# Optimization experiments

Hardware: AMD Instinct MI355X
Metric: run time of the kernel (lower is better)

The kernel has to match this reference:

```python
import jax, jax.numpy as jnp
import numpy as np

B, S, D, H, N = 2, 2048, 768, 12, 128  # batch, seq_len, d_model, n_heads, num_segments
EPS_LN = 1e-5


def _layer_norm(x, g, b):
    m = x.mean(-1, keepdims=True)
    v = ((x - m) ** 2).mean(-1, keepdims=True)
    return (x - m) / jnp.sqrt(v + EPS_LN) * g + b


def _mha(q, k, v, Wqkv, bqkv, Wo, bo, n_heads):
    """torch.nn.MultiheadAttention (batch_first), returns (out, head-averaged attn)."""
    d = q.shape[-1]
    dh = d // n_heads
    Wq, Wk, Wv = jnp.split(Wqkv, 3, axis=0)
    bq, bk, bv = jnp.split(bqkv, 3)
    qh = (q @ Wq.T + bq).reshape(q.shape[0], q.shape[1], n_heads, dh)
    kh = (k @ Wk.T + bk).reshape(k.shape[0], k.shape[1], n_heads, dh)
    vh = (v @ Wv.T + bv).reshape(v.shape[0], v.shape[1], n_heads, dh)
    scores = jnp.einsum('bqhd,bkhd->bhqk', qh, kh) / jnp.sqrt(jnp.asarray(dh, q.dtype))
    attn = jax.nn.softmax(scores, axis=-1)                      # [B,H,Sq,Sk]
    out = jnp.einsum('bhqk,bkhd->bqhd', attn, vh).reshape(q.shape[0], q.shape[1], d)
    return out @ Wo.T + bo, attn.mean(axis=1)                   # attn avg over heads


def _aggregate(x, w, seg):  # per-batch: weighted mean of tokens into N segments
    num = jax.ops.segment_sum(w[:, None] * x, seg, num_segments=N)
    den = jax.ops.segment_sum(w, seg, num_segments=N)
    return num / (den[:, None] + 1e-8)


def setup_inputs() -> dict:
    key = jax.random.key(0)
    ks = jax.random.split(key, 16)
    s = 0.02
    inp = {
        'hidden_states': jax.random.normal(ks[0], (B, S, D), jnp.float32),
        'token_to_segment': jnp.sort(jax.random.randint(ks[1], (B, S), 0, N), axis=-1),
        # token_attention (shared for node-level self-attn in the adjacency=None branch)
        'Wqkv_t': jax.random.normal(ks[2], (3 * D, D), jnp.float32) * s,
        'bqkv_t': jnp.zeros((3 * D,), jnp.float32),
        'Wo_t': jax.random.normal(ks[3], (D, D), jnp.float32) * s,
        'bo_t': jnp.zeros((D,), jnp.float32),
        # cross_attention
        'Wqkv_c': jax.random.normal(ks[4], (3 * D, D), jnp.float32) * s,
        'bqkv_c': jnp.zeros((3 * D,), jnp.float32),
        'Wo_c': jax.random.normal(ks[5], (D, D), jnp.float32) * s,
        'bo_c': jnp.zeros((D,), jnp.float32),
        # layer norms
        'g_tok': jnp.ones((D,), jnp.float32),
        'b_tok': jnp.zeros((D,), jnp.float32),
        'g_node': jnp.ones((D,), jnp.float32),
        'b_node': jnp.zeros((D,), jnp.float32),
        # output projection
        'W_out': jax.random.normal(ks[6], (D, D), jnp.float32) * s,
        'b_out': jnp.zeros((D,), jnp.float32),
    }
    return inp


def reference(hidden_states, token_to_segment, Wqkv_t, bqkv_t, Wo_t, bo_t,
              Wqkv_c, bqkv_c, Wo_c, bo_c, g_tok, b_tok, g_node, b_node,
              W_out, b_out):
    hs = hidden_states
    # token-level self-attention + residual norm
    tok_attn_out, tok_attn = _mha(hs, hs, hs, Wqkv_t, bqkv_t, Wo_t, bo_t, H)
    token_output = _layer_norm(hs + tok_attn_out, g_tok, b_tok)
    # token -> node attention-weighted scatter aggregation
    w = tok_attn.mean(axis=1)  # [B,S] attention received per token
    node_emb = jax.vmap(_aggregate)(token_output, w, token_to_segment)  # [B,N,D]
    # node-level self-attention (reuses token_attention weights; adjacency=None path)
    node_out, node_attn = _mha(node_emb, node_emb, node_emb, Wqkv_t, bqkv_t, Wo_t, bo_t, H)
    node_emb = _layer_norm(node_emb + node_out, g_node, b_node)
    # cross-attention: tokens attend to nodes
    cross_out, cross_w = _mha(token_output, node_emb, node_emb, Wqkv_c, bqkv_c, Wo_c, bo_c, H)
    token_output = token_output + cross_out
    # node -> token gather + additive combine
    gathered = jnp.take_along_axis(node_emb, token_to_segment[:, :, None], axis=1)  # [B,S,D]
    enhanced = token_output + gathered
    output = enhanced @ W_out.T + b_out
    return output, node_emb, tok_attn, node_attn, cross_w
```

## Files before the change

### kernel.cpp

```cpp
#include <hip/hip_runtime.h>
#include <cstdint>

#define B_ 2
#define S_ 2048
#define D_ 768
#define H_ 12
#define DH_ 64
#define N_ 128

typedef unsigned short u16;
typedef unsigned int u32;
typedef unsigned long long u64;
typedef __attribute__((ext_vector_type(8))) short short8;
typedef __attribute__((ext_vector_type(4))) float f32x4;

#define MFMA16(a, b, c) __builtin_amdgcn_mfma_f32_16x16x32_bf16(a, b, c, 0, 0, 0)

__device__ inline u16 f2bf(float f) {
  union { float f; u32 u; } v; v.f = f;
  u32 r = v.u + 0x7FFFu + ((v.u >> 16) & 1u);
  return (u16)(r >> 16);
}
__device__ inline u32 pk2(float a, float b) {
  return (u32)f2bf(a) | ((u32)f2bf(b) << 16);
}
__device__ inline u32 cvtpk(float lo, float hi) {
  u32 r;
  asm("v_cvt_pk_bf16_f32 %0, %1, %2" : "=v"(r) : "v"(lo), "v"(hi));
  return r;
}
__device__ inline float bf2f(u16 h) {
  union { u32 u; float f; } v; v.u = ((u32)h) << 16;
  return v.f;
}
__device__ inline float wredmax(float v) {
  #pragma unroll
  for (int o = 32; o > 0; o >>= 1) v = fmaxf(v, __shfl_down(v, o));
  return v;
}
__device__ inline float wredsum(float v) {
  #pragma unroll
  for (int o = 32; o > 0; o >>= 1) v += __shfl_down(v, o);
  return v;
}
__device__ inline void async_lds16(const u16* g, u16* l) {
  __builtin_amdgcn_global_load_lds((const __attribute__((address_space(1))) void*)g,
                                   (__attribute__((address_space(3))) void*)l, 16, 0, 0);
}

__global__ void conv_bf16(const float* __restrict__ in, u16* __restrict__ outp, int n8) {
  int i = blockIdx.x * 256 + threadIdx.x;
  if (i >= n8) return;
  const float4* p = (const float4*)(in + (size_t)i * 8);
  float4 a = p[0], b = p[1];
  uint4 u;
  u.x = pk2(a.x, a.y); u.y = pk2(a.z, a.w); u.z = pk2(b.x, b.y); u.w = pk2(b.z, b.w);
  *(uint4*)(outp + (size_t)i * 8) = u;
}

template <int OUT_BF16>
__global__ __launch_bounds__(256) void gemm_bf16(
    const u16* __restrict__ A, int lda,
    const u16* __restrict__ W, int ldb,
    const float* __restrict__ bias,
    void* __restrict__ Cout, int ldc, int K) {
  __shared__ u16 As[128 * 32];
  __shared__ u16 Ws[128 * 32];
  const int tid = threadIdx.x;
  const int m0 = blockIdx.y * 128, n0 = blockIdx.x * 128;
  const int w = tid >> 6, lane = tid & 63;
  const int msub = (w & 1) * 64, nsub = (w >> 1) * 64;
  const int lrow = lane & 15, quad = lane >> 4;
  const int e0 = tid * 8;
  const int r0 = e0 >> 5, c0 = e0 & 31;
  const int e1 = e0 + 2048;
  const int r1 = e1 >> 5, c1 = e1 & 31;
  const u16* Ag0 = A + (size_t)(m0 + r0) * lda + c0;
  const u16* Ag1 = A + (size_t)(m0 + r1) * lda + c1;
  const u16* Wg0 = W + (size_t)(n0 + r0) * ldb + c0;
  const u16* Wg1 = W + (size_t)(n0 + r1) * ldb + c1;
  u16* AsB0 = As + (w << 9);
  u16* AsB1 = As + 2048 + (w << 9);
  u16* WsB0 = Ws + (w << 9);
  u16* WsB1 = Ws + 2048 + (w << 9);
  f32x4 zero = {0.f, 0.f, 0.f, 0.f};
  f32x4 acc[4][4];
  #pragma unroll
  for (int i = 0; i < 4; i++)
    #pragma unroll
    for (int j = 0; j < 4; j++) acc[i][j] = zero;
  for (int k0 = 0; k0 < K; k0 += 32) {
    __syncthreads();
    async_lds16(Ag0 + k0, AsB0);
    async_lds16(Ag1 + k0, AsB1);
    async_lds16(Wg0 + k0, WsB0);
    async_lds16(Wg1 + k0, WsB1);
    __syncthreads();
    short8 af[4], bf[4];
    #pragma unroll
    for (int i = 0; i < 4; i++)
      af[i] = *(const short8*)(As + (msub + i * 16 + lrow) * 32 + quad * 8);
    #pragma unroll
    for (int j = 0; j < 4; j++)
      bf[j] = *(const short8*)(Ws + (nsub + j * 16 + lrow) * 32 + quad * 8);
    #pragma unroll
    for (int i = 0; i < 4; i++)
      #pragma unroll
      for (int j = 0; j < 4; j++)
        acc[i][j] = MFMA16(af[i], bf[j], acc[i][j]);
  }
  #pragma unroll
  for (int i = 0; i < 4; i++) {
    #pragma unroll
    for (int j = 0; j < 4; j++) {
      int col = n0 + nsub + j * 16 + lrow;
      float bv = bias ? bias[col] : 0.f;
      #pragma unroll
      for (int r = 0; r < 4; r++) {
        int row = m0 + msub + i * 16 + quad * 4 + r;
        float val = acc[i][j][r] + bv;
        if (OUT_BF16) ((u16*)Cout)[(size_t)row * ldc + col] = f2bf(val);
        else ((float*)Cout)[(size_t)row * ldc + col] = val;
      }
    }
  }
}

__global__ __launch_bounds__(256) void transpose_v(const u16* __restrict__ qkv, u16* __restrict__ VT) {
  __shared__ u16 t[64][72];
  const int z = blockIdx.y, b = z / 12, h = z - b * 12;
  const int s0 = blockIdx.x * 64;
  const int tid = threadIdx.x;
  {
    int r = tid >> 2, dp = (tid & 3) * 16;
    const u16* src = qkv + (size_t)b * 2048 * 2304 + (size_t)(s0 + r) * 2304 + 1536 + h * 64 + dp;
    *(uint4*)&t[r][dp] = *(const uint4*)src;
    *(uint4*)&t[r][dp + 8] = *(const uint4*)(src + 8);
  }
  __syncthreads();
  int d = tid >> 2, sp = (tid & 3) * 16;
  u16 vals[16];
  #pragma unroll
  for (int i = 0; i < 16; i++) vals[i] = t[sp + i][d];
  u16* dst = VT + ((size_t)z * 64 + d) * 2048 + s0 + sp;
  *(uint4*)dst = *(uint4*)&vals[0];
  *(uint4*)(dst + 8) = *(uint4*)&vals[8];
}

__global__ __launch_bounds__(512) void fused_tok_attn(
    const u16* __restrict__ qkv, const u16* __restrict__ VT,
    float* __restrict__ amF, u16* __restrict__ amH, u16* __restrict__ attnout) {
  __shared__ u16 pbuf[8 * 2 * 16 * 264];
  __shared__ float lred[8][2][16];
  __shared__ float obuf[2][2][16][66];
  const int tid = threadIdx.x;
  const int w = tid >> 6, lane = tid & 63;
  const int lrow = lane & 15, quad = lane >> 4;
  const int lid = blockIdx.x;
  const int xcd = lid & 7;
  const int combo = xcd >> 1;
  const int b = combo >> 1, z = combo & 1;
  const int q0 = (((lid >> 3) << 1) + (xcd & 1)) << 5;
  const int h0 = z * 6;
  const u16* qp = qkv + (size_t)b * 2048 * 2304;
  const u16* kp = qp + 768;
  const int strip = w * 256;
  const int jj = w & 3, sh = w >> 2;
  u16* ob = attnout + (size_t)b * 2048 * 768 + (size_t)q0 * 768;
  u16* pbA = pbuf + (w * 2 + 0) * 16 * 264;
  u16* pbB = pbuf + (w * 2 + 1) * 16 * 264;
  f32x4 zero = {0.f, 0.f, 0.f, 0.f};
  float amreg[2][8][8];
  #pragma unroll
  for (int g = 0; g < 2; g++)
    #pragma unroll
    for (int c = 0; c < 8; c++)
      #pragma unroll
      for (int e = 0; e < 8; e++) amreg[g][c][e] = 0.f;
  for (int hh = 0; hh < 6; hh++) {
    const int h = h0 + hh;
    const u16* qhA = qp + (size_t)(q0 + lrow) * 2304 + h * 64 + quad * 8;
    const u16* qhB = qp + (size_t)(q0 + 16 + lrow) * 2304 + h * 64 + quad * 8;
    short8 qfA0 = *(const short8*)qhA;
    short8 qfA1 = *(const short8*)(qhA + 32);
    short8 qfB0 = *(const short8*)qhB;
    short8 qfB1 = *(const short8*)(qhB + 32);
    float lsumA = 0.f, lsumB = 0.f;
    #pragma unroll
    for (int t = 0; t < 16; t++) {
      const u16* kh = kp + (size_t)(strip + t * 16 + lrow) * 2304 + h * 64 + quad * 8;
      short8 kf0 = *(const short8*)kh;
      short8 kf1 = *(const short8*)(kh + 32);
      f32x4 svA = zero, svB = zero;
      svA = MFMA16(kf0, qfA0, svA);
      svA = MFMA16(kf1, qfA1, svA);
      svB = MFMA16(kf0, qfB0, svB);
      svB = MFMA16(kf1, qfB1, svB);
      float a0 = __expf(svA[0] * 0.125f);
      float a1 = __expf(svA[1] * 0.125f);
      float a2 = __expf(svA[2] * 0.125f);
      float a3 = __expf(svA[3] * 0.125f);
      float b0 = __expf(svB[0] * 0.125f);
      float b1 = __expf(svB[1] * 0.125f);
      float b2 = __expf(svB[2] * 0.125f);
      float b3 = __expf(svB[3] * 0.125f);
      lsumA += (a0 + a1) + (a2 + a3);
      lsumB += (b0 + b1) + (b2 + b3);
      u32 wA0 = cvtpk(a0, a1), wA1 = cvtpk(a2, a3);
      u32 wB0 = cvtpk(b0, b1), wB1 = cvtpk(b2, b3);
      *(u64*)(pbA + lrow * 264 + t * 16 + quad * 4) = (u64)wA0 | ((u64)wA1 << 32);
      *(u64*)(pbB + lrow * 264 + t * 16 + quad * 4) = (u64)wB0 | ((u64)wB1 << 32);
    }
    lsumA += __shfl_xor(lsumA, 16);
    lsumA += __shfl_xor(lsumA, 32);
    lsumB += __shfl_xor(lsumB, 16);
    lsumB += __shfl_xor(lsumB, 32);
    if (lane < 16) { lred[w][0][lane] = lsumA; lred[w][1][lane] = lsumB; }
    __syncthreads();
    float invqA, invqB;
    float inv4A[4], inv4B[4];
    {
      float sA = 0.f, sB = 0.f;
      #pragma unroll
      for (int w2 = 0; w2 < 8; w2++) { sA += lred[w2][0][lrow]; sB += lred[w2][1][lrow]; }
      invqA = 1.f / sA; invqB = 1.f / sB;
      #pragma unroll
      for (int r = 0; r < 4; r++) {
        float rA = 0.f, rB = 0.f;
        #pragma unroll
        for (int w2 = 0; w2 < 8; w2++) {
          rA += lred[w2][0][quad * 4 + r];
          rB += lred[w2][1][quad * 4 + r];
        }
        inv4A[r] = 1.f / rA; inv4B[r] = 1.f / rB;
      }
    }
    #pragma unroll
    for (int c = 0; c < 8; c++) {
      short8 pfa = *(const short8*)(pbA + lrow * 264 + c * 32 + quad * 8);
      short8 pfb = *(const short8*)(pbB + lrow * 264 + c * 32 + quad * 8);
      #pragma unroll
      for (int e = 0; e < 8; e++) {
        amreg[0][c][e] += bf2f((u16)pfa[e]) * invqA;
        amreg[1][c][e] += bf2f((u16)pfb[e]) * invqB;
      }
    }
    f32x4 oA = zero, oB = zero;
    {
      const u16* vtp = VT + (size_t)(b * 12 + h) * 64 * 2048;
      const u16* vbase = vtp + (size_t)(jj * 16 + lrow) * 2048 + sh * 1024 + quad * 8;
      #pragma unroll
      for (int cc = 0; cc < 32; cc++) {
        short8 vf = *(const short8*)(vbase + cc * 32);
        const u16* pba = pbuf + (((4 * sh + (cc >> 3)) * 2 + 0) * 16 * 264) + lrow * 264 + (cc & 7) * 32 + quad * 8;
        const u16* pbb = pba + 16 * 264;
        oA = MFMA16(*(const short8*)pba, vf, oA);
        oB = MFMA16(*(const short8*)pbb, vf, oB);
      }
    }
    #pragma unroll
    for (int r = 0; r < 4; r++) {
      obuf[0][sh][quad * 4 + r][jj * 16 + lrow] = oA[r] * inv4A[r];
      obuf[1][sh][quad * 4 + r][jj * 16 + lrow] = oB[r] * inv4B[r];
    }
    __syncthreads();
    #pragma unroll
    for (int ee = 0; ee < 4; ee++) {
      int e2 = tid + ee * 512;
      int row = e2 >> 6, col = e2 & 63;
      int g = row >> 4, rr = row & 15;
      float s = obuf[g][0][rr][col] + obuf[g][1][rr][col];
      ob[(size_t)row * 768 + h * 64 + col] = f2bf(s);
    }
  }
  if (z == 0) {
    #pragma unroll
    for (int g = 0; g < 2; g++) {
      float* ar = amF + ((size_t)b * 2048 + q0 + g * 16 + lrow) * 2048 + strip;
      #pragma unroll
      for (int c = 0; c < 8; c++) {
        float4 v0 = {amreg[g][c][0], amreg[g][c][1], amreg[g][c][2], amreg[g][c][3]};
        float4 v1 = {amreg[g][c][4], amreg[g][c][5], amreg[g][c][6], amreg[g][c][7]};
        *(float4*)(ar + c * 32 + quad * 8) = v0;
        *(float4*)(ar + c * 32 + quad * 8 + 4) = v1;
      }
    }
  } else {
    #pragma unroll
    for (int g = 0; g < 2; g++) {
      u16* ar = amH + ((size_t)b * 2048 + q0 + g * 16 + lrow) * 2048 + strip;
      #pragma unroll
      for (int c = 0; c < 8; c++) {
        uint4 u;
        u.x = pk2(amreg[g][c][0], amreg[g][c][1]);
        u.y = pk2(amreg[g][c][2], amreg[g][c][3]);
        u.z = pk2(amreg[g][c][4], amreg[g][c][5]);
        u.w = pk2(amreg[g][c][6], amreg[g][c][7]);
        *(uint4*)(ar + c * 32 + quad * 8) = u;
      }
    }
  }
}

__global__ void combine_am(float* __restrict__ amF, const u16* __restrict__ amH) {
  size_t i = ((size_t)blockIdx.x * 256 + threadIdx.x) * 8;
  float4 a0 = *(float4*)(amF + i);
  float4 a1 = *(float4*)(amF + i + 4);
  uint4 hb = *(const uint4*)(amH + i);
  const float c12 = 1.f / 12.f;
  float4 r0, r1;
  r0.x = (a0.x + bf2f((u16)(hb.x & 0xffff))) * c12;
  r0.y = (a0.y + bf2f((u16)(hb.x >> 16))) * c12;
  r0.z = (a0.z + bf2f((u16)(hb.y & 0xffff))) * c12;
  r0.w = (a0.w + bf2f((u16)(hb.y >> 16))) * c12;
  r1.x = (a1.x + bf2f((u16)(hb.z & 0xffff))) * c12;
  r1.y = (a1.y + bf2f((u16)(hb.z >> 16))) * c12;
  r1.z = (a1.z + bf2f((u16)(hb.w & 0xffff))) * c12;
  r1.w = (a1.w + bf2f((u16)(hb.w >> 16))) * c12;
  *(float4*)(amF + i) = r0;
  *(float4*)(amF + i + 4) = r1;
}

__global__ __launch_bounds__(256) void qk_mfma(
    const u16* __restrict__ Q, int ldq, long qbs,
    const u16* __restrict__ Kp, int ldk, long kbs,
    float* __restrict__ S, long szs, int Sk, int nh, float scale) {
  __shared__ u16 Qs[128 * 72];
  __shared__ u16 Ks[128 * 72];
  const int tid = threadIdx.x;
  const int z = blockIdx.z, bb = z / nh, h = z - bb * nh;
  const u16* qp = Q + (size_t)bb * qbs + h * 64;
  const u16* kp = Kp + (size_t)bb * kbs + h * 64;
  float* sp = S + (size_t)z * szs;
  const int m0 = blockIdx.y * 128, n0 = blockIdx.x * 128;
  const int w = tid >> 6, lane = tid & 63;
  const int msub = (w & 1) * 64, nsub = (w >> 1) * 64;
  const int lrow = lane & 15, quad = lane >> 4;
  const int srow = tid >> 1, shalf = tid & 1;
  {
    const uint4* qg = (const uint4*)(qp + (size_t)(m0 + srow) * ldq + shalf * 32);
    const uint4* kg = (const uint4*)(kp + (size_t)(n0 + srow) * ldk + shalf * 32);
    uint4* qd = (uint4*)(Qs + srow * 72 + shalf * 32);
    uint4* kd = (uint4*)(Ks + srow * 72 + shalf * 32);
    #pragma unroll
    for (int u = 0; u < 4; u++) { qd[u] = qg[u]; kd[u] = kg[u]; }
  }
  __syncthreads();
  f32x4 zero = {0.f, 0.f, 0.f, 0.f};
  f32x4 acc[4][4];
  #pragma unroll
  for (int i = 0; i < 4; i++)
    #pragma unroll
    for (int j = 0; j < 4; j++) acc[i][j] = zero;
  #pragma unroll
  for (int ks = 0; ks < 2; ks++) {
    short8 af[4], bf[4];
    #pragma unroll
    for (int i = 0; i < 4; i++)
      af[i] = *(const short8*)(Qs + (msub + i * 16 + lrow) * 72 + ks * 32 + quad * 8);
    #pragma unroll
    for (int j = 0; j < 4; j++)
      bf[j] = *(const short8*)(Ks + (nsub + j * 16 + lrow) * 72 + ks * 32 + quad * 8);
    #pragma unroll
    for (int i = 0; i < 4; i++)
      #pragma unroll
      for (int j = 0; j < 4; j++)
        acc[i][j] = MFMA16(af[i], bf[j], acc[i][j]);
  }
  #pragma unroll
  for (int i = 0; i < 4; i++)
    #pragma unroll
    for (int j = 0; j < 4; j++) {
      int col = n0 + nsub + j * 16 + lrow;
      #pragma unroll
      for (int r = 0; r < 4; r++) {
        int row = m0 + msub + i * 16 + quad * 4 + r;
        sp[(size_t)row * Sk + col] = acc[i][j][r] * scale;
      }
    }
}

__global__ __launch_bounds__(128) void softmax_small(
    float* __restrict__ Sc, float* __restrict__ wout, int Sq) {
  const int q = blockIdx.x, b = blockIdx.y, tid = threadIdx.x;
  const int w = tid >> 6, lane = tid & 63;
  __shared__ float red[2];
  float am = 0.f;
  const size_t plane = (size_t)Sq * 128;
  for (int h = 0; h < 12; h++) {
    const int z = b * 12 + h;
    float* row = Sc + (size_t)z * plane + (size_t)q * 128;
    float v = row[tid];
    float m = wredmax(v);
    if (lane == 0) red[w] = m;
    __syncthreads();
    m = fmaxf(red[0], red[1]);
    float e = __expf(v - m);
    float s = wredsum(e);
    __syncthreads();
    if (lane == 0) red[w] = s;
    __syncthreads();
    float p = e / (red[0] + red[1]);
    ((u16*)(Sc + (size_t)z * plane))[(size_t)q * 256 + tid] = f2bf(p);
    am += p;
    __syncthreads();
  }
  wout[((size_t)b * Sq + q) * 128 + tid] = am * (1.f / 12.f);
}

__global__ __launch_bounds__(256) void pv_small(
    const u16* __restrict__ Pb, long pzs,
    const u16* __restrict__ KVb, int ldv, long vbs, int vhoff,
    u16* __restrict__ Outb, long obs) {
  __shared__ u16 Ps[128 * 40];
  __shared__ u16 Vs[64 * 40];
  const int tid = threadIdx.x;
  const int z = blockIdx.y, b = z / 12, h = z - b * 12;
  const u16* Pp = Pb + (size_t)z * pzs;
  const u16* Vp = KVb + (size_t)b * vbs + vhoff + h * 64;
  u16* Op = Outb + (size_t)b * obs + h * 64;
  const int m0 = blockIdx.x * 128;
  const int w = tid >> 6, lane = tid & 63;
  const int msub = w * 32;
  const int lrow = lane & 15, quad = lane >> 4;
  const int srow = tid >> 1, shalf = tid & 1;
  const int vk = tid >> 3, vn = (tid & 7) * 8;
  f32x4 zero = {0.f, 0.f, 0.f, 0.f};
  f32x4 acc[2][4];
  #pragma unroll
  for (int i = 0; i < 2; i++)
    #pragma unroll
    for (int j = 0; j < 4; j++) acc[i][j] = zero;
  #pragma unroll
  for (int k0 = 0; k0 < 128; k0 += 32) {
    uint4 pa = *(const uint4*)(Pp + (size_t)(m0 + srow) * 256 + k0 + shalf * 16);
    uint4 pb2 = *(const uint4*)(Pp + (size_t)(m0 + srow) * 256 + k0 + shalf * 16 + 8);
    uint4 vv = *(const uint4*)(Vp + (size_t)(k0 + vk) * ldv + vn);
    __syncthreads();
    *(uint4*)(Ps + srow * 40 + shalf * 16) = pa;
    *(uint4*)(Ps + srow * 40 + shalf * 16 + 8) = pb2;
    const u16* vs = (const u16*)&vv;
    #pragma unroll
    for (int u = 0; u < 8; u++) Vs[(vn + u) * 40 + vk] = vs[u];
    __syncthreads();
    short8 af[2], bf[4];
    #pragma unroll
    for (int i = 0; i < 2; i++)
      af[i] = *(const short8*)(Ps + (msub + i * 16 + lrow) * 40 + quad * 8);
    #pragma unroll
    for (int j = 0; j < 4; j++)
      bf[j] = *(const short8*)(Vs + (j * 16 + lrow) * 40 + quad * 8);
    #pragma unroll
    for (int i = 0; i < 2; i++)
      #pragma unroll
      for (int j = 0; j < 4; j++)
        acc[i][j] = MFMA16(af[i], bf[j], acc[i][j]);
  }
  #pragma unroll
  for (int i = 0; i < 2; i++)
    #pragma unroll
    for (int j = 0; j < 4; j++) {
      int col = j * 16 + lrow;
      #pragma unroll
      for (int r = 0; r < 4; r++) {
        int row = m0 + msub + i * 16 + quad * 4 + r;
        Op[(size_t)row * D_ + col] = f2bf(acc[i][j][r]);
      }
    }
}

__global__ void ln_kernel(const float* __restrict__ x1, const float* __restrict__ x2,
                          const float* __restrict__ g, const float* __restrict__ bt,
                          float* __restrict__ outp, u16* __restrict__ outbf) {
  const int row = blockIdx.x;
  const int tid = threadIdx.x;
  __shared__ float red[8];
  float v[3];
  #pragma unroll
  for (int j = 0; j < 3; j++) {
    int c = tid + j * 256;
    v[j] = x1[(size_t)row * D_ + c] + x2[(size_t)row * D_ + c];
  }
  float s = v[0] + v[1] + v[2];
  s = wredsum(s);
  int wid = tid >> 6, lane = tid & 63;
  if (lane == 0) red[wid] = s;
  __syncthreads();
  float mean = (red[0] + red[1] + red[2] + red[3]) / 768.f;
  float d0 = v[0] - mean, d1 = v[1] - mean, d2 = v[2] - mean;
  float q = d0 * d0 + d1 * d1 + d2 * d2;
  q = wredsum(q);
  if (lane == 0) red[4 + wid] = q;
  __syncthreads();
  float var = (red[4] + red[5] + red[6] + red[7]) / 768.f;
  float inv = rsqrtf(var + 1e-5f);
  #pragma unroll
  for (int j = 0; j < 3; j++) {
    int c = tid + j * 256;
    float val = (v[j] - mean) * inv * g[c] + bt[c];
    outp[(size_t)row * D_ + c] = val;
    if (outbf) outbf[(size_t)row * D_ + c] = f2bf(val);
  }
}

__global__ void colmean_part(const float* __restrict__ ta, float* __restrict__ part) {
  int b = blockIdx.y, z = blockIdx.z;
  int k = blockIdx.x * 256 + threadIdx.x;
  const float* p = ta + (size_t)b * S_ * S_ + (size_t)z * 256 * S_ + k;
  float s = 0.f;
  #pragma unroll 8
  for (int q = 0; q < 256; q++) s += p[(size_t)q * S_];
  part[((size_t)z * B_ + b) * S_ + k] = s;
}

__global__ void colmean_final(const float* __restrict__ part, float* __restrict__ w) {
  int b = blockIdx.y;
  int k = blockIdx.x * 256 + threadIdx.x;
  float s = 0.f;
  #pragma unroll
  for (int z = 0; z < 8; z++) s += part[((size_t)z * B_ + b) * S_ + k];
  w[b * S_ + k] = s * (1.f / (float)S_);
}

__global__ void aggregate_kernel(const float* __restrict__ x, const float* __restrict__ w,
                                 const int* __restrict__ seg, float* __restrict__ outp,
                                 u16* __restrict__ outbf) {
  const int b = blockIdx.y, n = blockIdx.x;
  const int* sg = seg + b * S_;
  int l = 0, rr = S_;
  while (l < rr) { int mid = (l + rr) >> 1; if (sg[mid] < n) l = mid + 1; else rr = mid; }
  const int lo = l;
  rr = S_;
  while (l < rr) { int mid = (l + rr) >> 1; if (sg[mid] < n + 1) l = mid + 1; else rr = mid; }
  const int hi = l;
  const int tid = threadIdx.x;
  float acc[3] = {0.f, 0.f, 0.f};
  float den = 0.f;
  for (int s = lo; s < hi; s++) {
    float ww = w[b * S_ + s];
    den += ww;
    const float* xr = x + (size_t)(b * S_ + s) * D_;
    #pragma unroll
    for (int j = 0; j < 3; j++) acc[j] += ww * xr[tid + j * 256];
  }
  float invd = 1.f / (den + 1e-8f);
  size_t ro = (size_t)(b * N_ + n) * D_;
  #pragma unroll
  for (int j = 0; j < 3; j++) {
    float val = acc[j] * invd;
    outp[ro + tid + j * 256] = val;
    outbf[ro + tid + j * 256] = f2bf(val);
  }
}

__global__ void enhanced_kernel(const float* __restrict__ tokout, const float* __restrict__ crossp,
                                const float* __restrict__ nodeemb, const int* __restrict__ seg,
                                u16* __restrict__ outbf) {
  int g8 = blockIdx.x * 256 + threadIdx.x;
  int bs = g8 / 96, d0 = (g8 - bs * 96) * 8;
  int b = bs >> 11;
  int n = seg[bs];
  const float* t = tokout + (size_t)bs * D_ + d0;
  const float* cp = crossp + (size_t)bs * D_ + d0;
  const float* ne = nodeemb + (size_t)(b * N_ + n) * D_ + d0;
  float4 a0 = *(const float4*)t, a1 = *(const float4*)(t + 4);
  float4 b0 = *(const float4*)cp, b1 = *(const float4*)(cp + 4);
  float4 c0 = *(const float4*)ne, c1 = *(const float4*)(ne + 4);
  uint4 u;
  u.x = pk2(a0.x + b0.x + c0.x, a0.y + b0.y + c0.y);
  u.y = pk2(a0.z + b0.z + c0.z, a0.w + b0.w + c0.w);
  u.z = pk2(a1.x + b1.x + c1.x, a1.y + b1.y + c1.y);
  u.w = pk2(a1.z + b1.z + c1.z, a1.w + b1.w + c1.w);
  *(uint4*)(outbf + (size_t)g8 * 8) = u;
}

extern "C" void kernel_launch(void* const* d_in, const int* in_sizes, int n_in,
                              void* d_out, int out_size, void* d_ws, size_t ws_size,
                              hipStream_t stream) {
  const float* hs     = (const float*)d_in[0];
  const int*   t2s    = (const int*)d_in[1];
  const float* Wqkv_t = (const float*)d_in[2];
  const float* bqkv_t = (const float*)d_in[3];
  const float* Wo_t   = (const float*)d_in[4];
  const float* bo_t   = (const float*)d_in[5];
  const float* Wqkv_c = (const float*)d_in[6];
  const float* bqkv_c = (const float*)d_in[7];
  const float* Wo_c   = (const float*)d_in[8];
  const float* bo_c   = (const float*)d_in[9];
  const float* g_tok  = (const float*)d_in[10];
  const float* b_tok  = (const float*)d_in[11];
  const float* g_node = (const float*)d_in[12];
  const float* b_node = (const float*)d_in[13];
  const float* W_out  = (const float*)d_in[14];
  const float* b_out  = (const float*)d_in[15];

  float* ws = (float*)d_ws;
  u16*   qkvbf       = (u16*)ws;
  u16*   enh_bf      = (u16*)ws;
  u16*   crossqbf    = (u16*)(ws + 1572864);
  u16*   crossattn_bf= (u16*)(ws + 3145728);
  float* R1 = ws + 4718592;
  u16*   hs_bf   = (u16*)R1;
  u16*   wqkvt1  = (u16*)(R1 + 1572864);
  u16*   VT      = (u16*)R1;
  u16*   amh     = (u16*)(R1 + 4194304);
  float* projbuf = R1;
  float* Snode   = R1;
  u16*   wqkvt2  = (u16*)(R1 + 4000000);
  u16*   wot     = (u16*)(R1 + 6291456);
  u16*   wqkvc   = (u16*)R1;
  u16*   woc     = (u16*)(R1 + 6291456);
  u16*   wout    = (u16*)(R1 + 6586368);
  float* Scross  = R1;
  float* crossproj = R1;
  float* R2 = ws + 13107200;
  u16*   attnout_bf = (u16*)R2;
  u16*   tokout_bf  = (u16*)R2;
  float* wvec       = R2 + 1572864;
  float* colpart    = R2 + 1576960;
  float* nodepre    = R2 + 1609728;
  float* nodeproj   = R2 + 1806336;
  u16*   nodepre_bf = (u16*)(R2 + 2002944);
  u16*   nodeattn_bf= (u16*)(R2 + 2101248);
  u16*   nodeemb_bf = (u16*)(R2 + 2199552);
  u16*   nodeqkvbf  = (u16*)(R2 + 2297856);
  u16*   crosskvbf  = (u16*)(R2 + 2592768);
  float* tokout = ws + 16252928;

  float* outp       = (float*)d_out;
  float* o_output   = outp;
  float* o_nodeemb  = outp + 3145728;
  float* o_tokattn  = o_nodeemb + 196608;
  float* o_nodeattn = o_tokattn + 8388608;
  float* o_crossw   = o_nodeattn + 32768;

  conv_bf16<<<1536, 256, 0, stream>>>(hs, hs_bf, 393216);
  conv_bf16<<<864, 256, 0, stream>>>(Wqkv_t, wqkvt1, 221184);
  gemm_bf16<1><<<dim3(18, 32), 256, 0, stream>>>(hs_bf, 768, wqkvt1, 768, bqkv_t, qkvbf, 2304, 768);

  transpose_v<<<dim3(32, 24), 256, 0, stream>>>(qkvbf, VT);
  fused_tok_attn<<<256, 512, 0, stream>>>(qkvbf, VT, o_tokattn, amh, attnout_bf);
  combine_am<<<4096, 256, 0, stream>>>(o_tokattn, amh);

  conv_bf16<<<288, 256, 0, stream>>>(Wo_t, wot, 73728);
  gemm_bf16<0><<<dim3(6, 32), 256, 0, stream>>>(attnout_bf, 768, wot, 768, bo_t, projbuf, 768, 768);
  ln_kernel<<<4096, 256, 0, stream>>>(hs, projbuf, g_tok, b_tok, tokout, tokout_bf);

  colmean_part<<<dim3(8, 2, 8), 256, 0, stream>>>(o_tokattn, colpart);
  colmean_final<<<dim3(8, 2), 256, 0, stream>>>(colpart, wvec);
  aggregate_kernel<<<dim3(128, 2), 256, 0, stream>>>(tokout, wvec, t2s, nodepre, nodepre_bf);
  conv_bf16<<<864, 256, 0, stream>>>(Wqkv_t, wqkvt2, 221184);
  gemm_bf16<1><<<dim3(18, 2), 256, 0, stream>>>(nodepre_bf, 768, wqkvt2, 768, bqkv_t, nodeqkvbf, 2304, 768);
  qk_mfma<<<dim3(1, 1, 24), 256, 0, stream>>>(
      nodeqkvbf, 2304, (long)128 * 2304, nodeqkvbf + 768, 2304, (long)128 * 2304,
      Snode, 16384, 128, 12, 0.125f);
  softmax_small<<<dim3(128, 2), 128, 0, stream>>>(Snode, o_nodeattn, 128);
  pv_small<<<dim3(1, 24), 256, 0, stream>>>(
      (const u16*)Snode, 32768, nodeqkvbf, 2304, (long)128 * 2304, 1536,
      nodeattn_bf, (long)128 * 768);
  gemm_bf16<0><<<dim3(6, 2), 256, 0, stream>>>(nodeattn_bf, 768, wot, 768, bo_t, nodeproj, 768, 768);
  ln_kernel<<<256, 256, 0, stream>>>(nodepre, nodeproj, g_node, b_node, o_nodeemb, nodeemb_bf);

  conv_bf16<<<864, 256, 0, stream>>>(Wqkv_c, wqkvc, 221184);
  conv_bf16<<<288, 256, 0, stream>>>(Wo_c, woc, 73728);
  conv_bf16<<<288, 256, 0, stream>>>(W_out, wout, 73728);
  gemm_bf16<1><<<dim3(6, 32), 256, 0, stream>>>(tokout_bf, 768, wqkvc, 768, bqkv_c, crossqbf, 768, 768);
  gemm_bf16<1><<<dim3(12, 2), 256, 0, stream>>>(nodeemb_bf, 768, wqkvc + 768 * 768, 768, bqkv_c + 768,
                                                crosskvbf, 1536, 768);

  qk_mfma<<<dim3(1, 16, 24), 256, 0, stream>>>(
      crossqbf, 768, (long)2048 * 768, crosskvbf, 1536, (long)128 * 1536,
      Scross, 262144, 128, 12, 0.125f);
  softmax_small<<<dim3(2048, 2), 128, 0, stream>>>(Scross, o_crossw, 2048);
  pv_small<<<dim3(16, 24), 256, 0, stream>>>(
      (const u16*)Scross, 524288, crosskvbf, 1536, (long)128 * 1536, 768,
      crossattn_bf, (long)2048 * 768);

  gemm_bf16<0><<<dim3(6, 32), 256, 0, stream>>>(crossattn_bf, 768, woc, 768, bo_c, crossproj, 768, 768);
  enhanced_kernel<<<1536, 256, 0, stream>>>(tokout, crossproj, o_nodeemb, t2s, enh_bf);
  gemm_bf16<0><<<dim3(6, 32), 256, 0, stream>>>(enh_bf, 768, wout, 768, b_out, o_output, 768, 768);
}
```

Measured before the change: 556.9 us.

## Fuse small attention stages and fold head-average combine into column mean

Replaces the separate QK, softmax and PV kernels for node and cross attention with one attn_small kernel that keeps scores in registers and LDS and writes head-averaged weights directly. The combine pass over the token attention map is merged into the column-mean partial kernel, so the large fp32 map is read and written once fewer times. fused_tok_attn also gets a minimum-occupancy launch bound. The fused softmax omits the max subtraction, which risks overflow for large scores.

```diff
diff --git a/kernel.cpp b/kernel.cpp
--- a/kernel.cpp
+++ b/kernel.cpp
@@ -32,11 +32,6 @@
 __device__ inline float bf2f(u16 h) {
   union { u32 u; float f; } v; v.u = ((u32)h) << 16;
   return v.f;
-}
-__device__ inline float wredmax(float v) {
-  #pragma unroll
-  for (int o = 32; o > 0; o >>= 1) v = fmaxf(v, __shfl_down(v, o));
-  return v;
 }
 __device__ inline float wredsum(float v) {
   #pragma unroll
@@ -147,7 +142,7 @@
   *(uint4*)(dst + 8) = *(uint4*)&vals[8];
 }
 
-__global__ __launch_bounds__(512) void fused_tok_attn(
+__global__ __launch_bounds__(512, 2) void fused_tok_attn(
     const u16* __restrict__ qkv, const u16* __restrict__ VT,
     float* __restrict__ amF, u16* __restrict__ amH, u16* __restrict__ attnout) {
   __shared__ u16 pbuf[8 * 2 * 16 * 264];
@@ -302,171 +297,120 @@
   }
 }
 
-__global__ void combine_am(float* __restrict__ amF, const u16* __restrict__ amH) {
-  size_t i = ((size_t)blockIdx.x * 256 + threadIdx.x) * 8;
-  float4 a0 = *(float4*)(amF + i);
-  float4 a1 = *(float4*)(amF + i + 4);
-  uint4 hb = *(const uint4*)(amH + i);
+__global__ __launch_bounds__(256) void attn_small(
+    const u16* __restrict__ Qp, int ldq, long qbs,
+    const u16* __restrict__ Kp, int ldk, long kbs,
+    const u16* __restrict__ Vp,
+    u16* __restrict__ Outb, long obs,
+    float* __restrict__ wout, int Sq) {
+  __shared__ u16 pbuf[16][136];
+  __shared__ u16 Vs[64][136];
+  __shared__ float lred[4][16];
+  const int tid = threadIdx.x;
+  const int w = tid >> 6, lane = tid & 63;
+  const int lrow = lane & 15, quad = lane >> 4;
+  const int q0 = blockIdx.x * 16, b = blockIdx.y;
+  const u16* qb = Qp + (size_t)b * qbs;
+  const u16* kb = Kp + (size_t)b * kbs;
+  const u16* vb = Vp + (size_t)b * kbs;
+  u16* ob = Outb + (size_t)b * obs + (size_t)q0 * 768;
+  f32x4 zero = {0.f, 0.f, 0.f, 0.f};
+  float cw[2][4];
+  #pragma unroll
+  for (int t = 0; t < 2; t++)
+    #pragma unroll
+    for (int r = 0; r < 4; r++) cw[t][r] = 0.f;
+  for (int h = 0; h < 12; h++) {
+    __syncthreads();
+    #pragma unroll
+    for (int j = 0; j < 4; j++) {
+      int lin = tid * 32 + j * 8;
+      int s = lin >> 6, d = lin & 63;
+      uint4 vv = *(const uint4*)(vb + (size_t)s * ldk + h * 64 + d);
+      const u16* vsrc = (const u16*)&vv;
+      #pragma unroll
+      for (int u = 0; u < 8; u++) Vs[d + u][s] = vsrc[u];
+    }
+    const u16* qh = qb + (size_t)(q0 + lrow) * ldq + h * 64 + quad * 8;
+    short8 qf0 = *(const short8*)qh;
+    short8 qf1 = *(const short8*)(qh + 32);
+    float pr[2][4];
+    float lsum = 0.f;
+    #pragma unroll
+    for (int t = 0; t < 2; t++) {
+      const u16* kh = kb + (size_t)(w * 32 + t * 16 + lrow) * ldk + h * 64 + quad * 8;
+      short8 kf0 = *(const short8*)kh;
+      short8 kf1 = *(const short8*)(kh + 32);
+      f32x4 sv = zero;
+      sv = MFMA16(kf0, qf0, sv);
+      sv = MFMA16(kf1, qf1, sv);
+      #pragma unroll
+      for (int r = 0; r < 4; r++) {
+        float p = __expf(sv[r] * 0.125f);
+        pr[t][r] = p;
+        lsum += p;
+      }
+      u32 w0 = cvtpk(pr[t][0], pr[t][1]), w1 = cvtpk(pr[t][2], pr[t][3]);
+      *(u64*)(&pbuf[lrow][w * 32 + t * 16 + quad * 4]) = (u64)w0 | ((u64)w1 << 32);
+    }
+    lsum += __shfl_xor(lsum, 16);
+    lsum += __shfl_xor(lsum, 32);
+    if (lane < 16) lred[w][lane] = lsum;
+    __syncthreads();
+    float invq = 1.f / (lred[0][lrow] + lred[1][lrow] + lred[2][lrow] + lred[3][lrow]);
+    float inv4[4];
+    #pragma unroll
+    for (int r = 0; r < 4; r++)
+      inv4[r] = 1.f / (lred[0][quad * 4 + r] + lred[1][quad * 4 + r] +
+                       lred[2][quad * 4 + r] + lred[3][quad * 4 + r]);
+    #pragma unroll
+    for (int t = 0; t < 2; t++)
+      #pragma unroll
+      for (int r = 0; r < 4; r++) cw[t][r] += pr[t][r] * invq;
+    f32x4 oacc = zero;
+    #pragma unroll
+    for (int cc = 0; cc < 4; cc++) {
+      short8 pf = *(const short8*)(&pbuf[lrow][cc * 32 + quad * 8]);
+      short8 vf = *(const short8*)(&Vs[w * 16 + lrow][cc * 32 + quad * 8]);
+      oacc = MFMA16(pf, vf, oacc);
+    }
+    #pragma unroll
+    for (int r = 0; r < 4; r++)
+      ob[(size_t)(quad * 4 + r) * 768 + h * 64 + w * 16 + lrow] = f2bf(oacc[r] * inv4[r]);
+  }
+  float* wr = wout + ((size_t)b * Sq + q0 + lrow) * 128 + w * 32;
   const float c12 = 1.f / 12.f;
-  float4 r0, r1;
-  r0.x = (a0.x + bf2f((u16)(hb.x & 0xffff))) * c12;
-  r0.y = (a0.y + bf2f((u16)(hb.x >> 16))) * c12;
-  r0.z = (a0.z + bf2f((u16)(hb.y & 0xffff))) * c12;
-  r0.w = (a0.w + bf2f((u16)(hb.y >> 16))) * c12;
-  r1.x = (a1.x + bf2f((u16)(hb.z & 0xffff))) * c12;
-  r1.y = (a1.y + bf2f((u16)(hb.z >> 16))) * c12;
-  r1.z = (a1.z + bf2f((u16)(hb.w & 0xffff))) * c12;
-  r1.w = (a1.w + bf2f((u16)(hb.w >> 16))) * c12;
-  *(float4*)(amF + i) = r0;
-  *(float4*)(amF + i + 4) = r1;
-}
-
-__global__ __launch_bounds__(256) void qk_mfma(
-    const u16* __restrict__ Q, int ldq, long qbs,
-    const u16* __restrict__ Kp, int ldk, long kbs,
-    float* __restrict__ S, long szs, int Sk, int nh, float scale) {
-  __shared__ u16 Qs[128 * 72];
-  __shared__ u16 Ks[128 * 72];
-  const int tid = threadIdx.x;
-  const int z = blockIdx.z, bb = z / nh, h = z - bb * nh;
-  const u16* qp = Q + (size_t)bb * qbs + h * 64;
-  const u16* kp = Kp + (size_t)bb * kbs + h * 64;
-  float* sp = S + (size_t)z * szs;
-  const int m0 = blockIdx.y * 128, n0 = blockIdx.x * 128;
-  const int w = tid >> 6, lane = tid & 63;
-  const int msub = (w & 1) * 64, nsub = (w >> 1) * 64;
-  const int lrow = lane & 15, quad = lane >> 4;
-  const int srow = tid >> 1, shalf = tid & 1;
-  {
-    const uint4* qg = (const uint4*)(qp + (size_t)(m0 + srow) * ldq + shalf * 32);
-    const uint4* kg = (const uint4*)(kp + (size_t)(n0 + srow) * ldk + shalf * 32);
-    uint4* qd = (uint4*)(Qs + srow * 72 + shalf * 32);
-    uint4* kd = (uint4*)(Ks + srow * 72 + shalf * 32);
-    #pragma unroll
-    for (int u = 0; u < 4; u++) { qd[u] = qg[u]; kd[u] = kg[u]; }
-  }
-  __syncthreads();
-  f32x4 zero = {0.f, 0.f, 0.f, 0.f};
-  f32x4 acc[4][4];
-  #pragma unroll
-  for (int i = 0; i < 4; i++)
-    #pragma unroll
-    for (int j = 0; j < 4; j++) acc[i][j] = zero;
-  #pragma unroll
-  for (int ks = 0; ks < 2; ks++) {
-    short8 af[4], bf[4];
-    #pragma unroll
-    for (int i = 0; i < 4; i++)
-      af[i] = *(const short8*)(Qs + (msub + i * 16 + lrow) * 72 + ks * 32 + quad * 8);
-    #pragma unroll
-    for (int j = 0; j < 4; j++)
-      bf[j] = *(const short8*)(Ks + (nsub + j * 16 + lrow) * 72 + ks * 32 + quad * 8);
-    #pragma unroll
-    for (int i = 0; i < 4; i++)
-      #pragma unroll
-      for (int j = 0; j < 4; j++)
-        acc[i][j] = MFMA16(af[i], bf[j], acc[i][j]);
-  }
-  #pragma unroll
-  for (int i = 0; i < 4; i++)
-    #pragma unroll
-    for (int j = 0; j < 4; j++) {
-      int col = n0 + nsub + j * 16 + lrow;
-      #pragma unroll
-      for (int r = 0; r < 4; r++) {
-        int row = m0 + msub + i * 16 + quad * 4 + r;
-        sp[(size_t)row * Sk + col] = acc[i][j][r] * scale;
-      }
-    }
-}
-
-__global__ __launch_bounds__(128) void softmax_small(
-    float* __restrict__ Sc, float* __restrict__ wout, int Sq) {
-  const int q = blockIdx.x, b = blockIdx.y, tid = threadIdx.x;
-  const int w = tid >> 6, lane = tid & 63;
-  __shared__ float red[2];
-  float am = 0.f;
-  const size_t plane = (size_t)Sq * 128;
-  for (int h = 0; h < 12; h++) {
-    const int z = b * 12 + h;
-    float* row = Sc + (size_t)z * plane + (size_t)q * 128;
-    float v = row[tid];
-    float m = wredmax(v);
-    if (lane == 0) red[w] = m;
-    __syncthreads();
-    m = fmaxf(red[0], red[1]);
-    float e = __expf(v - m);
-    float s = wredsum(e);
-    __syncthreads();
-    if (lane == 0) red[w] = s;
-    __syncthreads();
-    float p = e / (red[0] + red[1]);
-    ((u16*)(Sc + (size_t)z * plane))[(size_t)q * 256 + tid] = f2bf(p);
-    am += p;
-    __syncthreads();
-  }
-  wout[((size_t)b * Sq + q) * 128 + tid] = am * (1.f / 12.f);
-}
-
-__global__ __launch_bounds__(256) void pv_small(
-    const u16* __restrict__ Pb, long pzs,
-    const u16* __restrict__ KVb, int ldv, long vbs, int vhoff,
-    u16* __restrict__ Outb, long obs) {
-  __shared__ u16 Ps[128 * 40];
-  __shared__ u16 Vs[64 * 40];
-  const int tid = threadIdx.x;
-  const int z = blockIdx.y, b = z / 12, h = z - b * 12;
-  const u16* Pp = Pb + (size_t)z * pzs;
-  const u16* Vp = KVb + (size_t)b * vbs + vhoff + h * 64;
-  u16* Op = Outb + (size_t)b * obs + h * 64;
-  const int m0 = blockIdx.x * 128;
-  const int w = tid >> 6, lane = tid & 63;
-  const int msub = w * 32;
-  const int lrow = lane & 15, quad = lane >> 4;
-  const int srow = tid >> 1, shalf = tid & 1;
-  const int vk = tid >> 3, vn = (tid & 7) * 8;
-  f32x4 zero = {0.f, 0.f, 0.f, 0.f};
-  f32x4 acc[2][4];
-  #pragma unroll
-  for (int i = 0; i < 2; i++)
-    #pragma unroll
-    for (int j = 0; j < 4; j++) acc[i][j] = zero;
-  #pragma unroll
-  for (int k0 = 0; k0 < 128; k0 += 32) {
-    uint4 pa = *(const uint4*)(Pp + (size_t)(m0 + srow) * 256 + k0 + shalf * 16);
-    uint4 pb2 = *(const uint4*)(Pp + (size_t)(m0 + srow) * 256 + k0 + shalf * 16 + 8);
-    uint4 vv = *(const uint4*)(Vp + (size_t)(k0 + vk) * ldv + vn);
-    __syncthreads();
-    *(uint4*)(Ps + srow * 40 + shalf * 16) = pa;
-    *(uint4*)(Ps + srow * 40 + shalf * 16 + 8) = pb2;
-    const u16* vs = (const u16*)&vv;
-    #pragma unroll
-    for (int u = 0; u < 8; u++) Vs[(vn + u) * 40 + vk] = vs[u];
-    __syncthreads();
-    short8 af[2], bf[4];
-    #pragma unroll
-    for (int i = 0; i < 2; i++)
-      af[i] = *(const short8*)(Ps + (msub + i * 16 + lrow) * 40 + quad * 8);
-    #pragma unroll
-    for (int j = 0; j < 4; j++)
-      bf[j] = *(const short8*)(Vs + (j * 16 + lrow) * 40 + quad * 8);
-    #pragma unroll
-    for (int i = 0; i < 2; i++)
-      #pragma unroll
-      for (int j = 0; j < 4; j++)
-        acc[i][j] = MFMA16(af[i], bf[j], acc[i][j]);
-  }
-  #pragma unroll
-  for (int i = 0; i < 2; i++)
-    #pragma unroll
-    for (int j = 0; j < 4; j++) {
-      int col = j * 16 + lrow;
-      #pragma unroll
-      for (int r = 0; r < 4; r++) {
-        int row = m0 + msub + i * 16 + quad * 4 + r;
-        Op[(size_t)row * D_ + col] = f2bf(acc[i][j][r]);
-      }
-    }
+  #pragma unroll
+  for (int t = 0; t < 2; t++)
+    #pragma unroll
+    for (int r = 0; r < 4; r++)
+      wr[t * 16 + quad * 4 + r] = cw[t][r] * c12;
+}
+
+__global__ void colmean_part(float* __restrict__ amF, const u16* __restrict__ amH,
+                             float* __restrict__ part) {
+  int b = blockIdx.y, z = blockIdx.z;
+  int k = blockIdx.x * 256 + threadIdx.x;
+  float* p = amF + (size_t)b * S_ * S_ + (size_t)z * 256 * S_ + k;
+  const u16* hp = amH + (size_t)b * S_ * S_ + (size_t)z * 256 * S_ + k;
+  const float c12 = 1.f / 12.f;
+  float s = 0.f;
+  #pragma unroll 8
+  for (int q = 0; q < 256; q++) {
+    float v = (p[(size_t)q * S_] + bf2f(hp[(size_t)q * S_])) * c12;
+    p[(size_t)q * S_] = v;
+    s += v;
+  }
+  part[((size_t)z * B_ + b) * S_ + k] = s;
+}
+
+__global__ void colmean_final(const float* __restrict__ part, float* __restrict__ w) {
+  int b = blockIdx.y;
+  int k = blockIdx.x * 256 + threadIdx.x;
+  float s = 0.f;
+  #pragma unroll
+  for (int z = 0; z < 8; z++) s += part[((size_t)z * B_ + b) * S_ + k];
+  w[b * S_ + k] = s * (1.f / (float)S_);
 }
 
 __global__ void ln_kernel(const float* __restrict__ x1, const float* __restrict__ x2,
@@ -501,25 +445,6 @@
     outp[(size_t)row * D_ + c] = val;
     if (outbf) outbf[(size_t)row * D_ + c] = f2bf(val);
   }
-}
-
-__global__ void colmean_part(const float* __restrict__ ta, float* __restrict__ part) {
-  int b = blockIdx.y, z = blockIdx.z;
-  int k = blockIdx.x * 256 + threadIdx.x;
-  const float* p = ta + (size_t)b * S_ * S_ + (size_t)z * 256 * S_ + k;
-  float s = 0.f;
-  #pragma unroll 8
-  for (int q = 0; q < 256; q++) s += p[(size_t)q * S_];
-  part[((size_t)z * B_ + b) * S_ + k] = s;
-}
-
-__global__ void colmean_final(const float* __restrict__ part, float* __restrict__ w) {
-  int b = blockIdx.y;
-  int k = blockIdx.x * 256 + threadIdx.x;
-  float s = 0.f;
-  #pragma unroll
-  for (int z = 0; z < 8; z++) s += part[((size_t)z * B_ + b) * S_ + k];
-  w[b * S_ + k] = s * (1.f / (float)S_);
 }
 
 __global__ void aggregate_kernel(const float* __restrict__ x, const float* __restrict__ w,
@@ -605,13 +530,11 @@
   u16*   VT      = (u16*)R1;
   u16*   amh     = (u16*)(R1 + 4194304);
   float* projbuf = R1;
-  float* Snode   = R1;
   u16*   wqkvt2  = (u16*)(R1 + 4000000);
   u16*   wot     = (u16*)(R1 + 6291456);
   u16*   wqkvc   = (u16*)R1;
   u16*   woc     = (u16*)(R1 + 6291456);
   u16*   wout    = (u16*)(R1 + 6586368);
-  float* Scross  = R1;
   float* crossproj = R1;
   float* R2 = ws + 13107200;
   u16*   attnout_bf = (u16*)R2;
@@ -640,24 +563,21 @@
 
   transpose_v<<<dim3(32, 24), 256, 0, stream>>>(qkvbf, VT);
   fused_tok_attn<<<256, 512, 0, stream>>>(qkvbf, VT, o_tokattn, amh, attnout_bf);
-  combine_am<<<4096, 256, 0, stream>>>(o_tokattn, amh);
+  colmean_part<<<dim3(8, 2, 8), 256, 0, stream>>>(o_tokattn, amh, colpart);
+  colmean_final<<<dim3(8, 2), 256, 0, stream>>>(colpart, wvec);
 
   conv_bf16<<<288, 256, 0, stream>>>(Wo_t, wot, 73728);
   gemm_bf16<0><<<dim3(6, 32), 256, 0, stream>>>(attnout_bf, 768, wot, 768, bo_t, projbuf, 768, 768);
   ln_kernel<<<4096, 256, 0, stream>>>(hs, projbuf, g_tok, b_tok, tokout, tokout_bf);
 
-  colmean_part<<<dim3(8, 2, 8), 256, 0, stream>>>(o_tokattn, colpart);
-  colmean_final<<<dim3(8, 2), 256, 0, stream>>>(colpart, wvec);
   aggregate_kernel<<<dim3(128, 2), 256, 0, stream>>>(tokout, wvec, t2s, nodepre, nodepre_bf);
   conv_bf16<<<864, 256, 0, stream>>>(Wqkv_t, wqkvt2, 221184);
   gemm_bf16<1><<<dim3(18, 2), 256, 0, stream>>>(nodepre_bf, 768, wqkvt2, 768, bqkv_t, nodeqkvbf, 2304, 768);
-  qk_mfma<<<dim3(1, 1, 24), 256, 0, stream>>>(
-      nodeqkvbf, 2304, (long)128 * 2304, nodeqkvbf + 768, 2304, (long)128 * 2304,
-      Snode, 16384, 128, 12, 0.125f);
-  softmax_small<<<dim3(128, 2), 128, 0, stream>>>(Snode, o_nodeattn, 128);
-  pv_small<<<dim3(1, 24), 256, 0, stream>>>(
-      (const u16*)Snode, 32768, nodeqkvbf, 2304, (long)128 * 2304, 1536,
-      nodeattn_bf, (long)128 * 768);
+  attn_small<<<dim3(8, 2), 256, 0, stream>>>(
+      nodeqkvbf, 2304, (long)128 * 2304,
+      nodeqkvbf + 768, 2304, (long)128 * 2304,
+      nodeqkvbf + 1536,
+      nodeattn_bf, (long)128 * 768, o_nodeattn, 128);
   gemm_bf16<0><<<dim3(6, 2), 256, 0, stream>>>(nodeattn_bf, 768, wot, 768, bo_t, nodeproj, 768, 768);
   ln_kernel<<<256, 256, 0, stream>>>(nodepre, nodeproj, g_node, b_node, o_nodeemb, nodeemb_bf);
 
@@ -668,13 +588,11 @@
   gemm_bf16<1><<<dim3(12, 2), 256, 0, stream>>>(nodeemb_bf, 768, wqkvc + 768 * 768, 768, bqkv_c + 768,
                                                 crosskvbf, 1536, 768);
 
-  qk_mfma<<<dim3(1, 16, 24), 256, 0, stream>>>(
-      crossqbf, 768, (long)2048 * 768, crosskvbf, 1536, (long)128 * 1536,
-      Scross, 262144, 128, 12, 0.125f);
-  softmax_small<<<dim3(2048, 2), 128, 0, stream>>>(Scross, o_crossw, 2048);
-  pv_small<<<dim3(16, 24), 256, 0, stream>>>(
-      (const u16*)Scross, 524288, crosskvbf, 1536, (long)128 * 1536, 768,
-      crossattn_bf, (long)2048 * 768);
+  attn_small<<<dim3(128, 2), 256, 0, stream>>>(
+      crossqbf, 768, (long)2048 * 768,
+      crosskvbf, 1536, (long)128 * 1536,
+      crosskvbf + 768,
+      crossattn_bf, (long)2048 * 768, o_crossw, 2048);
 
   gemm_bf16<0><<<dim3(6, 32), 256, 0, stream>>>(crossattn_bf, 768, woc, 768, bo_c, crossproj, 768, 768);
   enhanced_kernel<<<1536, 256, 0, stream>>>(tokout, crossproj, o_nodeemb, t2s, enh_bf);
```

Measured after the change: 552.8 us. About the same (-0.7%).
